# Kernel optimization log

Measured on AMD Instinct MI355X. Metric: run time of the kernel, lower is better.

Reference implementation:

```python
import math
import jax, jax.numpy as jnp
from jax import lax
import numpy as np

SPARSITY = 0.05
EMBEDDING_SIZE = 2048
BATCH = 32768


def setup_inputs() -> dict:
    key = jax.random.key(0)
    k0, k1, k2 = jax.random.split(key, 3)
    x = jax.random.normal(k0, (BATCH, 28, 28), dtype=jnp.float32)
    # conv: out=5, in=1, k=3, no bias (kaiming-ish scale)
    conv_w = jax.random.normal(k1, (5, 1, 3, 3), dtype=jnp.float32) * (1.0 / math.sqrt(9))
    bn_gamma = jnp.ones((5,), jnp.float32)
    bn_beta = jnp.zeros((5,), jnp.float32)
    bn_mean = jnp.zeros((5,), jnp.float32)
    bn_var = jnp.ones((5,), jnp.float32)
    # fc: [EMBEDDING_SIZE, 320], no bias
    fc_w = jax.random.normal(k2, (EMBEDDING_SIZE, 5 * 8 * 8), dtype=jnp.float32) * (1.0 / math.sqrt(320))
    return {"x": x, "conv_w": conv_w, "bn_gamma": bn_gamma, "bn_beta": bn_beta,
            "bn_mean": bn_mean, "bn_var": bn_var, "fc_w": fc_w}


def _kwta(z):
    # k-winners-take-all: top k_active entries per row -> 1, rest -> 0.
    k_active = math.ceil(SPARSITY * z.shape[1])
    topv, _ = lax.top_k(z, k_active)          # [B, k]
    thr = topv[:, -1:]                         # kth largest per row
    binary = (z >= thr).astype(z.dtype)
    # straight-through: forward = binary, backward = identity
    return z + lax.stop_gradient(binary - z)


def reference(x, conv_w, bn_gamma, bn_beta, bn_mean, bn_var, fc_w):
    h = x[:, None, :, :]  # [B,1,28,28]
    h = lax.conv_general_dilated(h, conv_w, window_strides=(1, 1), padding="VALID",
                                 dimension_numbers=("NCHW", "OIHW", "NCHW"))  # [B,5,26,26]
    inv_std = bn_gamma / jnp.sqrt(bn_var + 1e-5)
    h = (h - bn_mean[None, :, None, None]) * inv_std[None, :, None, None] + bn_beta[None, :, None, None]
    h = jnp.maximum(h, 0.0)
    # max_pool2d(kernel=3, stride=3), floor mode -> [B,5,8,8]
    h = lax.reduce_window(h, -jnp.inf, lax.max, (1, 1, 3, 3), (1, 1, 3, 3), "VALID")
    h = h.reshape(h.shape[0], -1)              # [B,320]
    z = h @ fc_w.T                             # [B,EMBEDDING_SIZE]
    return _kwta(z)
```

## Files before the change

### kernel.cpp

```cpp
#include <hip/hip_runtime.h>
#include <math.h>

#define BATCH 32768
#define EMB   2048
#define KDIM  320
#define KACT  103

#define BM 16
#define GTHREADS 1024

#define CIMG 16

typedef unsigned uint32x4 __attribute__((ext_vector_type(4)));

__global__ __launch_bounds__(256) void transpose_w_kernel(const float* __restrict__ W,
                                                          float* __restrict__ WT) {
  __shared__ float tile[32][33];
  const int k0 = blockIdx.x * 32;
  const int n0 = blockIdx.y * 32;
  const int tx = threadIdx.x;
  const int ty = threadIdx.y;
  for (int i = ty; i < 32; i += 8)
    tile[i][tx] = W[(size_t)(n0 + i) * KDIM + k0 + tx];
  __syncthreads();
  for (int i = ty; i < 32; i += 8)
    WT[(size_t)(k0 + i) * EMB + n0 + tx] = tile[tx][i];
}

__global__ __launch_bounds__(GTHREADS, 8) void fused_conv_gemm_topk(
    const float* __restrict__ x,
    const float* __restrict__ cw,
    const float* __restrict__ gamma,
    const float* __restrict__ beta,
    const float* __restrict__ mean,
    const float* __restrict__ var,
    float* __restrict__ HtW,
    const float* __restrict__ HtR,
    const float* __restrict__ WT,
    float* __restrict__ out) {
#pragma clang fp contract(off)
  __shared__ __attribute__((aligned(16))) float smem[18432];
  __shared__ float wv[45];
  __shared__ float inv_s[5], mu_s[5], be_s[5];
  __shared__ unsigned thr_s[BM];

  float* const xs = smem;
  float* const hs = smem + 12544;
  float* const zb = smem;

  const int t    = threadIdx.x;
  const int lane = t & 63;
  const int w    = t >> 6;
  const int b0   = blockIdx.x * CIMG;

  {
    const float4* src = (const float4*)(x + (size_t)b0 * 784);
    float4* dst = (float4*)xs;
    for (int i = t; i < CIMG * 196; i += GTHREADS) dst[i] = src[i];
  }
  if (t < 45) wv[t] = cw[t];
  if (t < 5) {
    inv_s[t] = gamma[t] / sqrtf(var[t] + 1e-5f);
    mu_s[t] = mean[t];
    be_s[t] = beta[t];
  }
  __syncthreads();

  {
    const int img = w;
    const float* xb = xs + img * 784;
    const int py = lane >> 3;
    const int px = lane & 7;

    float xr[5][5];
#pragma unroll
    for (int i = 0; i < 5; ++i)
#pragma unroll
      for (int j = 0; j < 5; ++j)
        xr[i][j] = xb[(3 * py + i) * 28 + 3 * px + j];

#pragma unroll
    for (int c = 0; c < 5; ++c) {
      float wr[9];
#pragma unroll
      for (int i = 0; i < 9; ++i) wr[i] = wv[c * 9 + i];
      const float inv = inv_s[c], mu = mu_s[c], be = be_s[c];
      float mx = -__builtin_huge_valf();
#pragma unroll
      for (int ry = 0; ry < 3; ++ry)
#pragma unroll
        for (int rx = 0; rx < 3; ++rx) {
          float s = 0.0f;
#pragma unroll
          for (int di = 0; di < 3; ++di)
#pragma unroll
            for (int dj = 0; dj < 3; ++dj)
              s = __builtin_fmaf(xr[ry + di][rx + dj], wr[di * 3 + dj], s);
          float t1 = s - mu;
          float t2 = t1 * inv;
          float t3 = t2 + be;
          mx = fmaxf(mx, t3);
        }
      hs[(c * 64 + lane) * 17 + img] = fmaxf(mx, 0.0f);
    }
  }
  __syncthreads();

  {
    float* dst = HtW + (size_t)blockIdx.x * (KDIM * CIMG);
    for (int i = t; i < KDIM * CIMG; i += GTHREADS) {
      const int k = i >> 4;
      const int img = i & 15;
      dst[i] = hs[k * 17 + img];
    }
  }
  __syncthreads();

  const int m0 = blockIdx.x * BM;
  const int nt = t * 2;

  float acc[BM][2];
#pragma unroll
  for (int m = 0; m < BM; ++m) {
    acc[m][0] = 0.0f;
    acc[m][1] = 0.0f;
  }

  const float* Ap = HtR + (size_t)blockIdx.x * (KDIM * BM);
  const float* wp = WT + nt;

#pragma unroll 4
  for (int k = 0; k < KDIM; ++k) {
    const float* ak = Ap + (size_t)k * BM;
    float av[BM];
#pragma unroll
    for (int m = 0; m < BM; ++m) av[m] = ak[m];
    const float2 bb = *(const float2*)(wp + (size_t)k * EMB);
#pragma unroll
    for (int m = 0; m < BM; ++m) {
      acc[m][0] = __builtin_fmaf(av[m], bb.x, acc[m][0]);
      acc[m][1] = __builtin_fmaf(av[m], bb.y, acc[m][1]);
    }
  }

  const int cW  = t >> 1;
  const int cWs = cW ^ ((cW >> 3) & 7);
  char* const zbase = (char*)zb;
  char* const wbase = zbase + (size_t)cWs * 16 + (size_t)(t & 1) * 8;

#pragma unroll
  for (int m = 0; m < 8; ++m)
    *(float2*)(wbase + (size_t)m * 8192) = *(const float2*)&acc[8 + m][0];
  __syncthreads();

  if (w >= 8) {
    const char* rowb = zbase + (size_t)(w - 8) * 8192;
    uint32x4 v4[8];
#pragma unroll
    for (int j = 0; j < 8; ++j) {
      const int c  = (lane << 3) | j;
      const int cs = c ^ (lane & 7);
      uint32x4 u = *(const uint32x4*)(rowb + (size_t)cs * 16);
#pragma unroll
      for (int e = 0; e < 4; ++e)
        u[e] = u[e] ^ (unsigned)(((int)u[e] >> 31) | 0x80000000);
      v4[j] = u;
      asm volatile("" : "+v"(v4[j]));
    }
    unsigned T = 0u;
    for (int b = 31; b >= 0; --b) {
      const unsigned cand = T | (1u << b);
      unsigned cnt = 0u;
#pragma unroll
      for (int j = 0; j < 8; ++j) {
        cnt += (unsigned)__popcll(__ballot(v4[j][0] >= cand));
        cnt += (unsigned)__popcll(__ballot(v4[j][1] >= cand));
        cnt += (unsigned)__popcll(__ballot(v4[j][2] >= cand));
        cnt += (unsigned)__popcll(__ballot(v4[j][3] >= cand));
      }
      if (cnt >= KACT) T = cand;
    }
    if (lane == 0) thr_s[w] = T;
  }
  __syncthreads();

#pragma unroll
  for (int m = 0; m < 8; ++m) {
    const float2 p = *(const float2*)(wbase + (size_t)m * 8192);
    const unsigned thr = thr_s[8 + m];
    unsigned ux = __float_as_uint(p.x); ux ^= (unsigned)(((int)ux >> 31) | 0x80000000);
    unsigned uy = __float_as_uint(p.y); uy ^= (unsigned)(((int)uy >> 31) | 0x80000000);
    float2 o;
    o.x = (ux >= thr) ? 1.0f : 0.0f;
    o.y = (uy >= thr) ? 1.0f : 0.0f;
    *(float2*)(out + (size_t)(m0 + 8 + m) * EMB + nt) = o;
  }
  __syncthreads();

#pragma unroll
  for (int m = 0; m < 8; ++m)
    *(float2*)(wbase + (size_t)m * 8192) = *(const float2*)&acc[m][0];
  __syncthreads();

  if (w < 8) {
    const char* rowb = zbase + (size_t)w * 8192;
    uint32x4 v4[8];
#pragma unroll
    for (int j = 0; j < 8; ++j) {
      const int c  = (lane << 3) | j;
      const int cs = c ^ (lane & 7);
      uint32x4 u = *(const uint32x4*)(rowb + (size_t)cs * 16);
#pragma unroll
      for (int e = 0; e < 4; ++e)
        u[e] = u[e] ^ (unsigned)(((int)u[e] >> 31) | 0x80000000);
      v4[j] = u;
      asm volatile("" : "+v"(v4[j]));
    }
    unsigned T = 0u;
    for (int b = 31; b >= 0; --b) {
      const unsigned cand = T | (1u << b);
      unsigned cnt = 0u;
#pragma unroll
      for (int j = 0; j < 8; ++j) {
        cnt += (unsigned)__popcll(__ballot(v4[j][0] >= cand));
        cnt += (unsigned)__popcll(__ballot(v4[j][1] >= cand));
        cnt += (unsigned)__popcll(__ballot(v4[j][2] >= cand));
        cnt += (unsigned)__popcll(__ballot(v4[j][3] >= cand));
      }
      if (cnt >= KACT) T = cand;
    }
    if (lane == 0) thr_s[w] = T;
  }
  __syncthreads();

#pragma unroll
  for (int m = 0; m < 8; ++m) {
    const float2 p = *(const float2*)(wbase + (size_t)m * 8192);
    const unsigned thr = thr_s[m];
    unsigned ux = __float_as_uint(p.x); ux ^= (unsigned)(((int)ux >> 31) | 0x80000000);
    unsigned uy = __float_as_uint(p.y); uy ^= (unsigned)(((int)uy >> 31) | 0x80000000);
    float2 o;
    o.x = (ux >= thr) ? 1.0f : 0.0f;
    o.y = (uy >= thr) ? 1.0f : 0.0f;
    *(float2*)(out + (size_t)(m0 + m) * EMB + nt) = o;
  }
}

extern "C" void kernel_launch(void* const* d_in, const int* in_sizes, int n_in,
                              void* d_out, int out_size, void* d_ws, size_t ws_size,
                              hipStream_t stream) {
  const float* x      = (const float*)d_in[0];
  const float* conv_w = (const float*)d_in[1];
  const float* gamma  = (const float*)d_in[2];
  const float* beta   = (const float*)d_in[3];
  const float* mean   = (const float*)d_in[4];
  const float* var    = (const float*)d_in[5];
  const float* fc_w   = (const float*)d_in[6];
  float* out = (float*)d_out;

  float* Ht = (float*)d_ws;
  float* WT = (float*)d_ws + (size_t)KDIM * BATCH;

  transpose_w_kernel<<<dim3(KDIM / 32, EMB / 32), dim3(32, 8), 0, stream>>>(fc_w, WT);
  fused_conv_gemm_topk<<<BATCH / CIMG, GTHREADS, 0, stream>>>(
      x, conv_w, gamma, beta, mean, var, Ht, Ht, WT, out);
}
```

Measured before the change: 824.0 us.

## Halve rows per block to 8 and do top-k threshold in one pass

Shrinks the per-block tile from 16 images/rows to 8, doubling the grid. The pooled conv output now goes straight to the global staging buffer without the shared transpose, and all 8 rows' scores fit in shared memory at once, so the two-phase top-k becomes a single pass. The score-to-sortable-key conversion moves before the shared store and is no longer repeated on readback. In exchange, each W column load is reused across only 8 rows instead of 16, which raises weight traffic per output, and half the warps sit idle during the conv and the threshold search.

```diff
diff --git a/kernel.cpp b/kernel.cpp
--- a/kernel.cpp
+++ b/kernel.cpp
@@ -6,10 +6,9 @@
 #define KDIM  320
 #define KACT  103
 
-#define BM 16
+#define BM 8
 #define GTHREADS 1024
-
-#define CIMG 16
+#define CIMG 8
 
 typedef unsigned uint32x4 __attribute__((ext_vector_type(4)));
 
@@ -39,14 +38,13 @@
     const float* __restrict__ WT,
     float* __restrict__ out) {
 #pragma clang fp contract(off)
-  __shared__ __attribute__((aligned(16))) float smem[18432];
+  __shared__ __attribute__((aligned(16))) unsigned smem[BM * EMB];
   __shared__ float wv[45];
   __shared__ float inv_s[5], mu_s[5], be_s[5];
   __shared__ unsigned thr_s[BM];
 
-  float* const xs = smem;
-  float* const hs = smem + 12544;
-  float* const zb = smem;
+  float* const xs = (float*)smem;
+  unsigned* const zb = smem;
 
   const int t    = threadIdx.x;
   const int lane = t & 63;
@@ -66,7 +64,7 @@
   }
   __syncthreads();
 
-  {
+  if (w < CIMG) {
     const int img = w;
     const float* xb = xs + img * 784;
     const int py = lane >> 3;
@@ -79,6 +77,7 @@
       for (int j = 0; j < 5; ++j)
         xr[i][j] = xb[(3 * py + i) * 28 + 3 * px + j];
 
+    float* dst = HtW + (size_t)blockIdx.x * (KDIM * BM);
 #pragma unroll
     for (int c = 0; c < 5; ++c) {
       float wr[9];
@@ -101,17 +100,7 @@
           float t3 = t2 + be;
           mx = fmaxf(mx, t3);
         }
-      hs[(c * 64 + lane) * 17 + img] = fmaxf(mx, 0.0f);
-    }
-  }
-  __syncthreads();
-
-  {
-    float* dst = HtW + (size_t)blockIdx.x * (KDIM * CIMG);
-    for (int i = t; i < KDIM * CIMG; i += GTHREADS) {
-      const int k = i >> 4;
-      const int img = i & 15;
-      dst[i] = hs[k * 17 + img];
+      dst[(c * 64 + lane) * BM + img] = fmaxf(mx, 0.0f);
     }
   }
   __syncthreads();
@@ -149,35 +138,38 @@
   char* const wbase = zbase + (size_t)cWs * 16 + (size_t)(t & 1) * 8;
 
 #pragma unroll
-  for (int m = 0; m < 8; ++m)
-    *(float2*)(wbase + (size_t)m * 8192) = *(const float2*)&acc[8 + m][0];
-  __syncthreads();
-
-  if (w >= 8) {
-    const char* rowb = zbase + (size_t)(w - 8) * 8192;
-    uint32x4 v4[8];
+  for (int m = 0; m < BM; ++m) {
+    unsigned ux = __float_as_uint(acc[m][0]);
+    unsigned uy = __float_as_uint(acc[m][1]);
+    uint2 u;
+    u.x = ux ^ (unsigned)(((int)ux >> 31) | 0x80000000);
+    u.y = uy ^ (unsigned)(((int)uy >> 31) | 0x80000000);
+    *(uint2*)(wbase + (size_t)m * 8192) = u;
+  }
+  __syncthreads();
+
+  if (w < BM) {
+    const char* rowb = zbase + (size_t)w * 8192;
+    unsigned v[32];
 #pragma unroll
     for (int j = 0; j < 8; ++j) {
       const int c  = (lane << 3) | j;
       const int cs = c ^ (lane & 7);
-      uint32x4 u = *(const uint32x4*)(rowb + (size_t)cs * 16);
-#pragma unroll
-      for (int e = 0; e < 4; ++e)
-        u[e] = u[e] ^ (unsigned)(((int)u[e] >> 31) | 0x80000000);
-      v4[j] = u;
-      asm volatile("" : "+v"(v4[j]));
-    }
+      const uint32x4 u = *(const uint32x4*)(rowb + (size_t)cs * 16);
+      v[j * 4 + 0] = u[0];
+      v[j * 4 + 1] = u[1];
+      v[j * 4 + 2] = u[2];
+      v[j * 4 + 3] = u[3];
+    }
+#pragma unroll
+    for (int j = 0; j < 32; ++j) asm volatile("" : "+v"(v[j]));
     unsigned T = 0u;
     for (int b = 31; b >= 0; --b) {
       const unsigned cand = T | (1u << b);
       unsigned cnt = 0u;
 #pragma unroll
-      for (int j = 0; j < 8; ++j) {
-        cnt += (unsigned)__popcll(__ballot(v4[j][0] >= cand));
-        cnt += (unsigned)__popcll(__ballot(v4[j][1] >= cand));
-        cnt += (unsigned)__popcll(__ballot(v4[j][2] >= cand));
-        cnt += (unsigned)__popcll(__ballot(v4[j][3] >= cand));
-      }
+      for (int j = 0; j < 32; ++j)
+        cnt += (unsigned)__popcll(__ballot(v[j] >= cand));
       if (cnt >= KACT) T = cand;
     }
     if (lane == 0) thr_s[w] = T;
@@ -185,63 +177,12 @@
   __syncthreads();
 
 #pragma unroll
-  for (int m = 0; m < 8; ++m) {
-    const float2 p = *(const float2*)(wbase + (size_t)m * 8192);
-    const unsigned thr = thr_s[8 + m];
-    unsigned ux = __float_as_uint(p.x); ux ^= (unsigned)(((int)ux >> 31) | 0x80000000);
-    unsigned uy = __float_as_uint(p.y); uy ^= (unsigned)(((int)uy >> 31) | 0x80000000);
+  for (int m = 0; m < BM; ++m) {
+    const uint2 u = *(const uint2*)(wbase + (size_t)m * 8192);
+    const unsigned thr = thr_s[m];
     float2 o;
-    o.x = (ux >= thr) ? 1.0f : 0.0f;
-    o.y = (uy >= thr) ? 1.0f : 0.0f;
-    *(float2*)(out + (size_t)(m0 + 8 + m) * EMB + nt) = o;
-  }
-  __syncthreads();
-
-#pragma unroll
-  for (int m = 0; m < 8; ++m)
-    *(float2*)(wbase + (size_t)m * 8192) = *(const float2*)&acc[m][0];
-  __syncthreads();
-
-  if (w < 8) {
-    const char* rowb = zbase + (size_t)w * 8192;
-    uint32x4 v4[8];
-#pragma unroll
-    for (int j = 0; j < 8; ++j) {
-      const int c  = (lane << 3) | j;
-      const int cs = c ^ (lane & 7);
-      uint32x4 u = *(const uint32x4*)(rowb + (size_t)cs * 16);
-#pragma unroll
-      for (int e = 0; e < 4; ++e)
-        u[e] = u[e] ^ (unsigned)(((int)u[e] >> 31) | 0x80000000);
-      v4[j] = u;
-      asm volatile("" : "+v"(v4[j]));
-    }
-    unsigned T = 0u;
-    for (int b = 31; b >= 0; --b) {
-      const unsigned cand = T | (1u << b);
-      unsigned cnt = 0u;
-#pragma unroll
-      for (int j = 0; j < 8; ++j) {
-        cnt += (unsigned)__popcll(__ballot(v4[j][0] >= cand));
-        cnt += (unsigned)__popcll(__ballot(v4[j][1] >= cand));
-        cnt += (unsigned)__popcll(__ballot(v4[j][2] >= cand));
-        cnt += (unsigned)__popcll(__ballot(v4[j][3] >= cand));
-      }
-      if (cnt >= KACT) T = cand;
-    }
-    if (lane == 0) thr_s[w] = T;
-  }
-  __syncthreads();
-
-#pragma unroll
-  for (int m = 0; m < 8; ++m) {
-    const float2 p = *(const float2*)(wbase + (size_t)m * 8192);
-    const unsigned thr = thr_s[m];
-    unsigned ux = __float_as_uint(p.x); ux ^= (unsigned)(((int)ux >> 31) | 0x80000000);
-    unsigned uy = __float_as_uint(p.y); uy ^= (unsigned)(((int)uy >> 31) | 0x80000000);
-    float2 o;
-    o.x = (ux >= thr) ? 1.0f : 0.0f;
-    o.y = (uy >= thr) ? 1.0f : 0.0f;
+    o.x = (u.x >= thr) ? 1.0f : 0.0f;
+    o.y = (u.y >= thr) ? 1.0f : 0.0f;
     *(float2*)(out + (size_t)(m0 + m) * EMB + nt) = o;
   }
 }
```

Result: slower. 2.088 ms (+153.4%).
